# Performance work log

Measured on AMD Instinct MI355X. Metric: run time of the kernel, lower is better.

## Reference

```python
import jax, jax.numpy as jnp
import numpy as np

B, S, EH, DH, A = 32, 2048, 512, 512, 512

def setup_inputs() -> dict:
    key = jax.random.key(0)
    k1, k2, k3, k4, k5 = jax.random.split(key, 5)
    decoder_hidden = jax.random.normal(k1, (2, B, DH), dtype=jnp.float32)
    encoder_outputs = jax.random.normal(k2, (B, S, 2 * EH), dtype=jnp.float32)
    # Linear weights stored as (in, out) for x @ W convention
    W = jax.random.normal(k3, (2 * EH, A), dtype=jnp.float32) / np.sqrt(2 * EH)
    U = jax.random.normal(k4, (2 * DH, A), dtype=jnp.float32) / np.sqrt(2 * DH)
    v = jax.random.normal(k5, (A, 1), dtype=jnp.float32) / np.sqrt(A)
    return {"decoder_hidden": decoder_hidden, "encoder_outputs": encoder_outputs,
            "W": W, "U": U, "v": v}

def reference(decoder_hidden, encoder_outputs, W, U, v):
    # (2, B, DH) -> (B, 2*DH), matching transpose(0,1).reshape(B, -1)
    b = decoder_hidden.shape[1]
    dh = jnp.transpose(decoder_hidden, (1, 0, 2)).reshape(b, -1)
    temp1 = jnp.einsum('bse,ea->bsa', encoder_outputs, W)   # (B, S, A)
    temp2 = dh @ U                                          # (B, A) — computed once, broadcast over S
    score = jnp.squeeze(jnp.tanh(temp1 + temp2[:, None, :]) @ v, -1)  # (B, S)
    attention_weights = jax.nn.softmax(score, axis=-1)      # (B, S)
    context_vector = jnp.einsum('bs,bse->be', attention_weights, encoder_outputs)[:, None, :]  # (B,1,2EH)
    return context_vector, attention_weights
```

## Files before the change

kernel.cpp:

```cpp
#include <hip/hip_runtime.h>
#include <hip/hip_bf16.h>

#define Bb 32
#define Ss 2048
#define Kk 1024
#define Aa 512

#define BM 128
#define BK 64
#define LDSA (BM * BK * 2)
#define LDSB (Aa * BK * 2)

typedef __bf16 bf16x8 __attribute__((ext_vector_type(8)));
typedef float f32x4 __attribute__((ext_vector_type(4)));

__device__ __forceinline__ unsigned short f2bf(float f) {
  unsigned u = __float_as_uint(f);
  u += 0x7FFFu + ((u >> 16) & 1u);
  return (unsigned short)(u >> 16);
}

__device__ __forceinline__ float tanh_fast(float x) {
  float e = __expf(2.f * x);
  return (e - 1.f) / (e + 1.f);
}

__global__ __launch_bounds__(256) void prep_wt(const float* __restrict__ W,
                                               unsigned short* __restrict__ Wt) {
  int idx = blockIdx.x * 256 + threadIdx.x;
  int a = idx & (Aa - 1);
  int k = idx >> 9;
  Wt[a * Kk + k] = f2bf(W[(size_t)k * Aa + a]);
}

__global__ __launch_bounds__(256) void t2_partial(const float* __restrict__ dh,
                                                  const float* __restrict__ U,
                                                  float* __restrict__ part) {
  const int b = blockIdx.x, kc = blockIdx.y, t = threadIdx.x;
  __shared__ float sdh[128];
  if (t < 128) {
    int k = kc * 128 + t;
    sdh[t] = dh[(k >> 9) * (Bb * 512) + b * 512 + (k & 511)];
  }
  __syncthreads();
#pragma unroll
  for (int h = 0; h < 2; ++h) {
    const int a = h * 256 + t;
    float s = 0.f;
#pragma unroll 8
    for (int kk = 0; kk < 128; ++kk) s += sdh[kk] * U[(size_t)(kc * 128 + kk) * Aa + a];
    part[(size_t)(b * 8 + kc) * Aa + a] = s;
  }
}

__global__ __launch_bounds__(256) void t2_reduce(const float* __restrict__ part,
                                                 float* __restrict__ t2) {
  const int idx = blockIdx.x * 256 + threadIdx.x;
  const int b = idx >> 9, a = idx & 511;
  float s = 0.f;
#pragma unroll
  for (int kc = 0; kc < 8; ++kc) s += part[(size_t)(b * 8 + kc) * Aa + a];
  t2[idx] = s;
}

__global__ __launch_bounds__(512) void score_gemm(const float* __restrict__ enc,
                                                  const unsigned short* __restrict__ Wt,
                                                  const float* __restrict__ t2,
                                                  const float* __restrict__ v,
                                                  float* __restrict__ score) {
  __shared__ __align__(16) char lds[LDSA + LDSB];
  char* sA = lds;
  char* sB = lds + LDSA;

  const int blk = blockIdx.x;
  const int b = blk >> 4, sc = blk & 15;
  const float* encBase = enc + (size_t)(b * Ss + sc * BM) * Kk;

  const int tid = threadIdx.x;
  const int lane = tid & 63;
  const int wid = tid >> 6;
  const int wy = wid >> 2, wx = wid & 3;

  const f32x4 zero = {0.f, 0.f, 0.f, 0.f};
  f32x4 acc[4][8];
#pragma unroll
  for (int i = 0; i < 4; ++i)
#pragma unroll
    for (int j = 0; j < 8; ++j) acc[i][j] = zero;

  for (int t = 0; t < Kk / BK; ++t) {
    const int k0 = t * BK;
#pragma unroll
    for (int p = 0; p < 4; ++p) {
      int f = tid + p * 512;
      int r = f >> 4;
      int c4 = (f & 15) << 2;
      const float4 src = *(const float4*)(encBase + r * Kk + k0 + c4);
      ushort4 w;
      w.x = f2bf(src.x); w.y = f2bf(src.y); w.z = f2bf(src.z); w.w = f2bf(src.w);
      int byteoff = r * (BK * 2) + ((c4 * 2) ^ ((r & 7) << 4));
      *(ushort4*)(sA + byteoff) = w;
    }
#pragma unroll
    for (int q = 0; q < 8; ++q) {
      int f = tid + q * 512;
      int a = f >> 3;
      int c8 = (f & 7) << 3;
      const uint4 src = *(const uint4*)(Wt + (size_t)a * Kk + k0 + c8);
      int byteoff = a * (BK * 2) + ((c8 * 2) ^ ((a & 7) << 4));
      *(uint4*)(sB + byteoff) = src;
    }
    __syncthreads();
#pragma unroll
    for (int kk = 0; kk < 2; ++kk) {
      bf16x8 af[4], bfr[8];
      const int kb = (kk * 32 + ((lane >> 4) << 3)) * 2;
#pragma unroll
      for (int mi = 0; mi < 4; ++mi) {
        int r = wy * 64 + mi * 16 + (lane & 15);
        af[mi] = *(const bf16x8*)(sA + r * (BK * 2) + (kb ^ ((r & 7) << 4)));
      }
#pragma unroll
      for (int ni = 0; ni < 8; ++ni) {
        int a = wx * 128 + ni * 16 + (lane & 15);
        bfr[ni] = *(const bf16x8*)(sB + a * (BK * 2) + (kb ^ ((a & 7) << 4)));
      }
#pragma unroll
      for (int mi = 0; mi < 4; ++mi)
#pragma unroll
        for (int ni = 0; ni < 8; ++ni)
          acc[mi][ni] = __builtin_amdgcn_mfma_f32_16x16x32_bf16(af[mi], bfr[ni], acc[mi][ni], 0, 0, 0);
    }
    __syncthreads();
  }

  float t2v[8], vv[8];
#pragma unroll
  for (int ni = 0; ni < 8; ++ni) {
    int c = wx * 128 + ni * 16 + (lane & 15);
    t2v[ni] = t2[b * Aa + c];
    vv[ni] = v[c];
  }
  float sp[4][4];
#pragma unroll
  for (int mi = 0; mi < 4; ++mi)
#pragma unroll
    for (int j = 0; j < 4; ++j) sp[mi][j] = 0.f;
#pragma unroll
  for (int mi = 0; mi < 4; ++mi)
#pragma unroll
    for (int ni = 0; ni < 8; ++ni)
#pragma unroll
      for (int j = 0; j < 4; ++j) {
        float x = acc[mi][ni][j] + t2v[ni];
        sp[mi][j] += vv[ni] * tanh_fast(x);
      }

  float* sbuf = (float*)lds;
#pragma unroll
  for (int mi = 0; mi < 4; ++mi)
#pragma unroll
    for (int j = 0; j < 4; ++j) {
      float s = sp[mi][j];
      s += __shfl_xor(s, 1);
      s += __shfl_xor(s, 2);
      s += __shfl_xor(s, 4);
      s += __shfl_xor(s, 8);
      if ((lane & 15) == 0) {
        int r = wy * 64 + mi * 16 + ((lane >> 4) << 2) + j;
        sbuf[r * 4 + wx] = s;
      }
    }
  __syncthreads();
  if (tid < BM) {
    float s = sbuf[tid * 4] + sbuf[tid * 4 + 1] + sbuf[tid * 4 + 2] + sbuf[tid * 4 + 3];
    score[b * Ss + sc * BM + tid] = s;
  }
}

__global__ __launch_bounds__(256) void softmax_k(float* __restrict__ aw) {
  const int b = blockIdx.x, t = threadIdx.x;
  __shared__ float red[8];
  float s[8];
  float m = -3.4e38f;
#pragma unroll
  for (int i = 0; i < 8; ++i) {
    s[i] = aw[b * Ss + t + i * 256];
    m = fmaxf(m, s[i]);
  }
#pragma unroll
  for (int off = 1; off < 64; off <<= 1) m = fmaxf(m, __shfl_xor(m, off));
  const int lane = t & 63, wv = t >> 6;
  if (lane == 0) red[wv] = m;
  __syncthreads();
  m = fmaxf(fmaxf(red[0], red[1]), fmaxf(red[2], red[3]));
  float e[8];
  float l = 0.f;
#pragma unroll
  for (int i = 0; i < 8; ++i) { e[i] = __expf(s[i] - m); l += e[i]; }
#pragma unroll
  for (int off = 1; off < 64; off <<= 1) l += __shfl_xor(l, off);
  if (lane == 0) red[4 + wv] = l;
  __syncthreads();
  l = red[4] + red[5] + red[6] + red[7];
  const float inv = 1.f / l;
#pragma unroll
  for (int i = 0; i < 8; ++i) aw[b * Ss + t + i * 256] = e[i] * inv;
}

__global__ __launch_bounds__(256) void ctx_partial(const float* __restrict__ enc,
                                                   const float* __restrict__ aw,
                                                   float* __restrict__ part) {
  const int b = blockIdx.x, ch = blockIdx.y, t = threadIdx.x;
  __shared__ float sw[64];
  const int s0 = ch * 64;
  if (t < 64) sw[t] = aw[b * Ss + s0 + t];
  __syncthreads();
  float ax = 0.f, ay = 0.f, az = 0.f, aww = 0.f;
  const float* ebase = enc + (size_t)(b * Ss + s0) * Kk + t * 4;
#pragma unroll 4
  for (int r = 0; r < 64; ++r) {
    const float4 ev = *(const float4*)(ebase + (size_t)r * Kk);
    const float w = sw[r];
    ax += w * ev.x; ay += w * ev.y; az += w * ev.z; aww += w * ev.w;
  }
  float4 o; o.x = ax; o.y = ay; o.z = az; o.w = aww;
  *(float4*)(part + (size_t)(b * 32 + ch) * Kk + t * 4) = o;
}

__global__ __launch_bounds__(256) void ctx_reduce(const float* __restrict__ part,
                                                  float* __restrict__ ctx) {
  const int idx = blockIdx.x * 256 + threadIdx.x;
  const int b = idx >> 10, e = idx & 1023;
  float s = 0.f;
#pragma unroll
  for (int ch = 0; ch < 32; ++ch) s += part[(size_t)(b * 32 + ch) * Kk + e];
  ctx[idx] = s;
}

extern "C" void kernel_launch(void* const* d_in, const int* in_sizes, int n_in,
                              void* d_out, int out_size, void* d_ws, size_t ws_size,
                              hipStream_t stream) {
  const float* dh  = (const float*)d_in[0];
  const float* enc = (const float*)d_in[1];
  const float* W   = (const float*)d_in[2];
  const float* U   = (const float*)d_in[3];
  const float* v   = (const float*)d_in[4];

  float* out_ctx = (float*)d_out;
  float* out_aw  = (float*)d_out + 32768;

  char* ws = (char*)d_ws;
  unsigned short* Wt = (unsigned short*)ws;
  float* t2p   = (float*)(ws + 1048576);
  float* t2    = (float*)(ws + 1048576 + 524288);
  float* cpart = (float*)(ws + 1048576 + 524288 + 65536);

  prep_wt<<<2048, 256, 0, stream>>>(W, Wt);
  t2_partial<<<dim3(32, 8), 256, 0, stream>>>(dh, U, t2p);
  t2_reduce<<<64, 256, 0, stream>>>(t2p, t2);
  score_gemm<<<512, 512, 0, stream>>>(enc, Wt, t2, v, out_aw);
  softmax_k<<<32, 256, 0, stream>>>(out_aw);
  ctx_partial<<<dim3(32, 32), 256, 0, stream>>>(enc, out_aw, cpart);
  ctx_reduce<<<128, 256, 0, stream>>>(cpart, out_ctx);
}
```

Before: 180.9 us.

## Double-buffer score GEMM LDS tiles with direct global-to-LDS weight loads

Measured after the change: 196.8 us. 1.09x slower.

```diff
diff --git a/kernel.cpp b/kernel.cpp
--- a/kernel.cpp
+++ b/kernel.cpp
@@ -8,8 +8,9 @@
 
 #define BM 128
 #define BK 64
-#define LDSA (BM * BK * 2)
-#define LDSB (Aa * BK * 2)
+#define NT (Kk / BK)
+#define ABUF (BM * BK * 2)
+#define BBUF (Aa * BK * 2)
 
 typedef __bf16 bf16x8 __attribute__((ext_vector_type(8)));
 typedef float f32x4 __attribute__((ext_vector_type(4)));
@@ -25,12 +26,29 @@
   return (e - 1.f) / (e + 1.f);
 }
 
+__device__ __forceinline__ void gll16(const void* g, void* l) {
+  __builtin_amdgcn_global_load_lds(
+      (const __attribute__((address_space(1))) unsigned int*)g,
+      (__attribute__((address_space(3))) unsigned int*)l, 16, 0, 0);
+}
+
 __global__ __launch_bounds__(256) void prep_wt(const float* __restrict__ W,
-                                               unsigned short* __restrict__ Wt) {
-  int idx = blockIdx.x * 256 + threadIdx.x;
-  int a = idx & (Aa - 1);
-  int k = idx >> 9;
-  Wt[a * Kk + k] = f2bf(W[(size_t)k * Aa + a]);
+                                               unsigned short* __restrict__ WtT) {
+  const int idx = blockIdx.x * 256 + threadIdx.x;
+  const int a = idx & 511;
+  const int g = idx >> 9;
+  const int k0 = g * 8;
+  const int t = k0 >> 6, kin = k0 & 63;
+  unsigned short u[8];
+#pragma unroll
+  for (int j = 0; j < 8; ++j) u[j] = f2bf(W[(size_t)(k0 + j) * Aa + a]);
+  uint4 pk;
+  pk.x = (unsigned)u[0] | ((unsigned)u[1] << 16);
+  pk.y = (unsigned)u[2] | ((unsigned)u[3] << 16);
+  pk.z = (unsigned)u[4] | ((unsigned)u[5] << 16);
+  pk.w = (unsigned)u[6] | ((unsigned)u[7] << 16);
+  const size_t byteoff = (size_t)t * 65536 + a * 128 + (((kin * 2) ^ ((a & 7) << 4)));
+  *(uint4*)((char*)WtT + byteoff) = pk;
 }
 
 __global__ __launch_bounds__(256) void t2_partial(const float* __restrict__ dh,
@@ -63,14 +81,65 @@
   t2[idx] = s;
 }
 
-__global__ __launch_bounds__(512) void score_gemm(const float* __restrict__ enc,
-                                                  const unsigned short* __restrict__ Wt,
-                                                  const float* __restrict__ t2,
-                                                  const float* __restrict__ v,
-                                                  float* __restrict__ score) {
-  __shared__ __align__(16) char lds[LDSA + LDSB];
-  char* sA = lds;
-  char* sB = lds + LDSA;
+#define STEP(curA, curB, nxtA, nxtB, T)                                         \
+  {                                                                             \
+    const int tn = (T) + 1;                                                     \
+    float4 av0, av1, av2, av3;                                                  \
+    if (tn < NT) {                                                              \
+      const float* eb = encBase + tn * BK;                                      \
+      av0 = *(const float4*)(eb + (size_t)(a_r0)      * Kk + a_c);              \
+      av1 = *(const float4*)(eb + (size_t)(a_r0 + 32) * Kk + a_c);              \
+      av2 = *(const float4*)(eb + (size_t)(a_r0 + 64) * Kk + a_c);              \
+      av3 = *(const float4*)(eb + (size_t)(a_r0 + 96) * Kk + a_c);              \
+      const char* gB = (const char*)WtT + (size_t)tn * 65536;                   \
+      _Pragma("unroll")                                                         \
+      for (int q = 0; q < 8; ++q)                                               \
+        gll16(gB + (tid + q * 512) * 16, (nxtB) + (tid + q * 512) * 16);        \
+    }                                                                           \
+    _Pragma("unroll")                                                           \
+    for (int kk = 0; kk < 2; ++kk) {                                            \
+      bf16x8 af[4], bfr[8];                                                     \
+      const int kb = (kk * 32 + ((lane >> 4) << 3)) * 2;                        \
+      _Pragma("unroll")                                                         \
+      for (int mi = 0; mi < 4; ++mi) {                                          \
+        int r = wy * 64 + mi * 16 + (lane & 15);                                \
+        af[mi] = *(const bf16x8*)((curA) + r * 128 + (kb ^ ((r & 7) << 4)));    \
+      }                                                                         \
+      _Pragma("unroll")                                                         \
+      for (int ni = 0; ni < 8; ++ni) {                                          \
+        int a = wx * 128 + ni * 16 + (lane & 15);                               \
+        bfr[ni] = *(const bf16x8*)((curB) + a * 128 + (kb ^ ((a & 7) << 4)));   \
+      }                                                                         \
+      _Pragma("unroll")                                                         \
+      for (int mi = 0; mi < 4; ++mi)                                            \
+        _Pragma("unroll")                                                       \
+        for (int ni = 0; ni < 8; ++ni)                                          \
+          acc[mi][ni] = __builtin_amdgcn_mfma_f32_16x16x32_bf16(af[mi], bfr[ni], acc[mi][ni], 0, 0, 0); \
+    }                                                                           \
+    if (tn < NT) {                                                              \
+      ushort4 w;                                                                \
+      w.x = f2bf(av0.x); w.y = f2bf(av0.y); w.z = f2bf(av0.z); w.w = f2bf(av0.w); \
+      *(ushort4*)((nxtA) + (a_r0)      * 128 + a_swz) = w;                      \
+      w.x = f2bf(av1.x); w.y = f2bf(av1.y); w.z = f2bf(av1.z); w.w = f2bf(av1.w); \
+      *(ushort4*)((nxtA) + (a_r0 + 32) * 128 + a_swz) = w;                      \
+      w.x = f2bf(av2.x); w.y = f2bf(av2.y); w.z = f2bf(av2.z); w.w = f2bf(av2.w); \
+      *(ushort4*)((nxtA) + (a_r0 + 64) * 128 + a_swz) = w;                      \
+      w.x = f2bf(av3.x); w.y = f2bf(av3.y); w.z = f2bf(av3.z); w.w = f2bf(av3.w); \
+      *(ushort4*)((nxtA) + (a_r0 + 96) * 128 + a_swz) = w;                      \
+    }                                                                           \
+    __syncthreads();                                                            \
+  }
+
+__global__ __launch_bounds__(512, 2) void score_gemm(const float* __restrict__ enc,
+                                                     const unsigned short* __restrict__ WtT,
+                                                     const float* __restrict__ t2,
+                                                     const float* __restrict__ v,
+                                                     float* __restrict__ score) {
+  __shared__ __align__(16) char lds[2 * (ABUF + BBUF)];
+  char* sA0 = lds;
+  char* sA1 = lds + ABUF;
+  char* sB0 = lds + 2 * ABUF;
+  char* sB1 = lds + 2 * ABUF + BBUF;
 
   const int blk = blockIdx.x;
   const int b = blk >> 4, sc = blk & 15;
@@ -81,6 +150,10 @@
   const int wid = tid >> 6;
   const int wy = wid >> 2, wx = wid & 3;
 
+  const int a_r0 = tid >> 4;
+  const int a_c = (tid & 15) << 2;
+  const int a_swz = (a_c * 2) ^ ((a_r0 & 7) << 4);
+
   const f32x4 zero = {0.f, 0.f, 0.f, 0.f};
   f32x4 acc[4][8];
 #pragma unroll
@@ -88,50 +161,29 @@
 #pragma unroll
     for (int j = 0; j < 8; ++j) acc[i][j] = zero;
 
-  for (int t = 0; t < Kk / BK; ++t) {
-    const int k0 = t * BK;
-#pragma unroll
-    for (int p = 0; p < 4; ++p) {
-      int f = tid + p * 512;
-      int r = f >> 4;
-      int c4 = (f & 15) << 2;
-      const float4 src = *(const float4*)(encBase + r * Kk + k0 + c4);
-      ushort4 w;
-      w.x = f2bf(src.x); w.y = f2bf(src.y); w.z = f2bf(src.z); w.w = f2bf(src.w);
-      int byteoff = r * (BK * 2) + ((c4 * 2) ^ ((r & 7) << 4));
-      *(ushort4*)(sA + byteoff) = w;
-    }
-#pragma unroll
-    for (int q = 0; q < 8; ++q) {
-      int f = tid + q * 512;
-      int a = f >> 3;
-      int c8 = (f & 7) << 3;
-      const uint4 src = *(const uint4*)(Wt + (size_t)a * Kk + k0 + c8);
-      int byteoff = a * (BK * 2) + ((c8 * 2) ^ ((a & 7) << 4));
-      *(uint4*)(sB + byteoff) = src;
-    }
+  {
+    float4 av0 = *(const float4*)(encBase + (size_t)(a_r0)      * Kk + a_c);
+    float4 av1 = *(const float4*)(encBase + (size_t)(a_r0 + 32) * Kk + a_c);
+    float4 av2 = *(const float4*)(encBase + (size_t)(a_r0 + 64) * Kk + a_c);
+    float4 av3 = *(const float4*)(encBase + (size_t)(a_r0 + 96) * Kk + a_c);
+#pragma unroll
+    for (int q = 0; q < 8; ++q)
+      gll16((const char*)WtT + (tid + q * 512) * 16, sB0 + (tid + q * 512) * 16);
+    ushort4 w;
+    w.x = f2bf(av0.x); w.y = f2bf(av0.y); w.z = f2bf(av0.z); w.w = f2bf(av0.w);
+    *(ushort4*)(sA0 + (a_r0)      * 128 + a_swz) = w;
+    w.x = f2bf(av1.x); w.y = f2bf(av1.y); w.z = f2bf(av1.z); w.w = f2bf(av1.w);
+    *(ushort4*)(sA0 + (a_r0 + 32) * 128 + a_swz) = w;
+    w.x = f2bf(av2.x); w.y = f2bf(av2.y); w.z = f2bf(av2.z); w.w = f2bf(av2.w);
+    *(ushort4*)(sA0 + (a_r0 + 64) * 128 + a_swz) = w;
+    w.x = f2bf(av3.x); w.y = f2bf(av3.y); w.z = f2bf(av3.z); w.w = f2bf(av3.w);
+    *(ushort4*)(sA0 + (a_r0 + 96) * 128 + a_swz) = w;
     __syncthreads();
-#pragma unroll
-    for (int kk = 0; kk < 2; ++kk) {
-      bf16x8 af[4], bfr[8];
-      const int kb = (kk * 32 + ((lane >> 4) << 3)) * 2;
-#pragma unroll
-      for (int mi = 0; mi < 4; ++mi) {
-        int r = wy * 64 + mi * 16 + (lane & 15);
-        af[mi] = *(const bf16x8*)(sA + r * (BK * 2) + (kb ^ ((r & 7) << 4)));
-      }
-#pragma unroll
-      for (int ni = 0; ni < 8; ++ni) {
-        int a = wx * 128 + ni * 16 + (lane & 15);
-        bfr[ni] = *(const bf16x8*)(sB + a * (BK * 2) + (kb ^ ((a & 7) << 4)));
-      }
-#pragma unroll
-      for (int mi = 0; mi < 4; ++mi)
-#pragma unroll
-        for (int ni = 0; ni < 8; ++ni)
-          acc[mi][ni] = __builtin_amdgcn_mfma_f32_16x16x32_bf16(af[mi], bfr[ni], acc[mi][ni], 0, 0, 0);
-    }
-    __syncthreads();
+  }
+
+  for (int t = 0; t < NT; t += 2) {
+    STEP(sA0, sB0, sA1, sB1, t)
+    STEP(sA1, sB1, sA0, sB0, t + 1)
   }
 
   float t2v[8], vv[8];
@@ -251,15 +303,15 @@
   float* out_aw  = (float*)d_out + 32768;
 
   char* ws = (char*)d_ws;
-  unsigned short* Wt = (unsigned short*)ws;
+  unsigned short* WtT = (unsigned short*)ws;
   float* t2p   = (float*)(ws + 1048576);
   float* t2    = (float*)(ws + 1048576 + 524288);
   float* cpart = (float*)(ws + 1048576 + 524288 + 65536);
 
-  prep_wt<<<2048, 256, 0, stream>>>(W, Wt);
+  prep_wt<<<256, 256, 0, stream>>>(W, WtT);
   t2_partial<<<dim3(32, 8), 256, 0, stream>>>(dh, U, t2p);
   t2_reduce<<<64, 256, 0, stream>>>(t2p, t2);
-  score_gemm<<<512, 512, 0, stream>>>(enc, Wt, t2, v, out_aw);
+  score_gemm<<<512, 512, 0, stream>>>(enc, WtT, t2, v, out_aw);
   softmax_k<<<32, 256, 0, stream>>>(out_aw);
   ctx_partial<<<dim3(32, 32), 256, 0, stream>>>(enc, out_aw, cpart);
   ctx_reduce<<<128, 256, 0, stream>>>(cpart, out_ctx);
```
